# Performance work log

Hardware: AMD Instinct MI355X
Metric: run time of the kernel (lower is better)

Reference implementation:

```python
import jax, jax.numpy as jnp
import numpy as np

N, C = 32768, 1230   # batch of samples, LVIS-scale class count
P = 0.8              # seesaw scale parameter
EPS = 1e-6


def setup_inputs() -> dict:
    key = jax.random.key(0)
    k1, k2, k3 = jax.random.split(key, 3)
    logits = jax.random.normal(k1, (N, C), dtype=jnp.float32)
    labels = jax.random.randint(k2, (N,), 0, C)
    targets = jax.nn.one_hot(labels, C, dtype=jnp.float32)  # one-hot float targets
    # class_counts: long-tailed per-class sample counts (buffer, built in __init__)
    counts = jax.random.randint(k3, (C,), 1, 100000).astype(jnp.float32)
    cond = counts[:, None] > counts[None, :]
    s = jnp.where(cond, (counts[None, :] / counts[:, None]) ** P,
                  jnp.ones((C, C), dtype=jnp.float32))
    return {"logits": logits, "targets": targets, "s": s}


def reference(logits, targets, s):
    # numerically-stable shift (matches torch: logits - max)
    logits = logits - jnp.max(logits, axis=-1, keepdims=True)
    e = jnp.exp(logits)                                   # [N, C]
    # denom[n,i] = sum_j (1 - t[n,j]) * s[i,j] * e[n,j] + e[n,i]
    # original code materializes [N, C, C]; algebraically this is a GEMM:
    denom = jnp.einsum('nj,ij->ni', (1.0 - targets) * e, s) + e
    sigma = e / (denom + EPS)
    loss = -(targets * jnp.log(sigma)).sum(-1)            # [N]
    return loss.mean()
```

## Files before the change

### kernel.cpp

```cpp
#include <hip/hip_runtime.h>
#include <math.h>


constexpr int N_ROWS = 32768;
constexpr int C_CLS  = 1230;
constexpr int C2     = C_CLS / 2;
constexpr int BLK    = 256;
constexpr int PER_T  = (C2 + BLK - 1) / BLK;
constexpr float EPS_F = 1e-6f;

__global__ __launch_bounds__(BLK) void seesaw_row_kernel(
    const float* __restrict__ logits,
    const float* __restrict__ targets,
    const float* __restrict__ s,
    float* __restrict__ row_loss)
{
    const int n    = blockIdx.x;
    const int t    = threadIdx.x;
    const int lane = t & 63;
    const int wv   = t >> 6;

    const float2* lrow = reinterpret_cast<const float2*>(logits  + (size_t)n * C_CLS);
    const float2* trow = reinterpret_cast<const float2*>(targets + (size_t)n * C_CLS);

    __shared__ float red_max[4];
    __shared__ float red_sum[4];
    __shared__ int   sh_label;
    __shared__ float sh_lval;

    float2 l[PER_T];
    float lmax = -INFINITY;
    #pragma unroll
    for (int k = 0; k < PER_T; ++k) {
        const int j2 = t + k * BLK;
        if (j2 < C2) {
            l[k] = lrow[j2];
            const float2 tv = trow[j2];
            lmax = fmaxf(lmax, fmaxf(l[k].x, l[k].y));
            if (tv.x > 0.5f) { sh_label = 2 * j2;     sh_lval = l[k].x; }
            if (tv.y > 0.5f) { sh_label = 2 * j2 + 1; sh_lval = l[k].y; }
        }
    }
    #pragma unroll
    for (int off = 32; off > 0; off >>= 1)
        lmax = fmaxf(lmax, __shfl_down(lmax, off));
    if (lane == 0) red_max[wv] = lmax;
    __syncthreads();
    const float m  = fmaxf(fmaxf(red_max[0], red_max[1]),
                           fmaxf(red_max[2], red_max[3]));
    const int   li = sh_label;
    const float lv = sh_lval;

    const float2* srow = reinterpret_cast<const float2*>(s + (size_t)li * C_CLS);
    const float sii = s[(size_t)li * C_CLS + li];
    float part = 0.0f;
    #pragma unroll
    for (int k = 0; k < PER_T; ++k) {
        const int j2 = t + k * BLK;
        if (j2 < C2) {
            const float2 sv = srow[j2];
            const float ex = expf(l[k].x - m);
            const float ey = expf(l[k].y - m);
            part = fmaf(sv.x, ex, part);
            part = fmaf(sv.y, ey, part);
        }
    }
    #pragma unroll
    for (int off = 32; off > 0; off >>= 1)
        part += __shfl_down(part, off);
    if (lane == 0) red_sum[wv] = part;
    __syncthreads();

    if (t == 0) {
        const float denom_full = red_sum[0] + red_sum[1] + red_sum[2] + red_sum[3];
        const float ei  = expf(lv - m);
        const float denom = denom_full - sii * ei + ei;
        row_loss[n] = logf(denom + EPS_F) - (lv - m);
    }
}

__global__ __launch_bounds__(BLK) void reduce_mean_kernel(
    const float* __restrict__ row_loss, float* __restrict__ out)
{
    const int t    = threadIdx.x;
    const int lane = t & 63;
    const int wv   = t >> 6;
    const float4* rl4 = reinterpret_cast<const float4*>(row_loss);
    constexpr int N4 = N_ROWS / 4;
    double acc = 0.0;
    #pragma unroll 4
    for (int i = t; i < N4; i += BLK) {
        const float4 v = rl4[i];
        acc += (double)v.x + (double)v.y + (double)v.z + (double)v.w;
    }
    #pragma unroll
    for (int off = 32; off > 0; off >>= 1)
        acc += __shfl_down(acc, off);
    __shared__ double red[4];
    if (lane == 0) red[wv] = acc;
    __syncthreads();
    if (t == 0) {
        const double tot = red[0] + red[1] + red[2] + red[3];
        out[0] = (float)(tot / (double)N_ROWS);
    }
}

extern "C" void kernel_launch(void* const* d_in, const int* in_sizes, int n_in,
                              void* d_out, int out_size, void* d_ws, size_t ws_size,
                              hipStream_t stream) {
    const float* logits  = (const float*)d_in[0];
    const float* targets = (const float*)d_in[1];
    const float* s       = (const float*)d_in[2];
    float* out      = (float*)d_out;
    float* row_loss = (float*)d_ws;

    seesaw_row_kernel<<<N_ROWS, BLK, 0, stream>>>(logits, targets, s, row_loss);
    reduce_mean_kernel<<<1, BLK, 0, stream>>>(row_loss, out);
}
```

Baseline: 333.3 us.

## Map one wavefront per row and drop block-level shared-memory reductions

Each 64-lane wavefront now processes a whole row, with four rows per block, so max, label and sum reductions use only xor shuffles with no __syncthreads or shared memory. The label index and value are gathered by summing shuffles (only one lane holds a nonzero), and the label is made wave-uniform with readfirstlane. expf and logf are replaced by the fast __expf and __logf intrinsics. Each lane now holds about 10 float2 values instead of 3, which raises register use and gives less parallelism per row.

```diff
diff --git a/kernel.cpp b/kernel.cpp
--- a/kernel.cpp
+++ b/kernel.cpp
@@ -6,7 +6,8 @@
 constexpr int C_CLS  = 1230;
 constexpr int C2     = C_CLS / 2;
 constexpr int BLK    = 256;
-constexpr int PER_T  = (C2 + BLK - 1) / BLK;
+constexpr int WPB    = BLK / 64;
+constexpr int ITERS  = (C2 + 63) / 64;
 constexpr float EPS_F = 1e-6f;
 
 __global__ __launch_bounds__(BLK) void seesaw_row_kernel(
@@ -15,67 +16,60 @@
     const float* __restrict__ s,
     float* __restrict__ row_loss)
 {
-    const int n    = blockIdx.x;
     const int t    = threadIdx.x;
     const int lane = t & 63;
     const int wv   = t >> 6;
+    const int n    = blockIdx.x * WPB + wv;
 
     const float2* lrow = reinterpret_cast<const float2*>(logits  + (size_t)n * C_CLS);
     const float2* trow = reinterpret_cast<const float2*>(targets + (size_t)n * C_CLS);
 
-    __shared__ float red_max[4];
-    __shared__ float red_sum[4];
-    __shared__ int   sh_label;
-    __shared__ float sh_lval;
+    float2 l[ITERS];
+    float lmax = -INFINITY;
+    float lval = 0.0f;
+    int   li   = 0;
 
-    float2 l[PER_T];
-    float lmax = -INFINITY;
     #pragma unroll
-    for (int k = 0; k < PER_T; ++k) {
-        const int j2 = t + k * BLK;
+    for (int it = 0; it < ITERS; ++it) {
+        const int j2 = lane + it * 64;
         if (j2 < C2) {
-            l[k] = lrow[j2];
+            l[it] = lrow[j2];
             const float2 tv = trow[j2];
-            lmax = fmaxf(lmax, fmaxf(l[k].x, l[k].y));
-            if (tv.x > 0.5f) { sh_label = 2 * j2;     sh_lval = l[k].x; }
-            if (tv.y > 0.5f) { sh_label = 2 * j2 + 1; sh_lval = l[k].y; }
+            lmax = fmaxf(lmax, fmaxf(l[it].x, l[it].y));
+            if (tv.x > 0.5f) { li = 2 * j2;     lval = l[it].x; }
+            if (tv.y > 0.5f) { li = 2 * j2 + 1; lval = l[it].y; }
+        }
+    }
+    #pragma unroll
+    for (int off = 32; off > 0; off >>= 1) {
+        lmax  = fmaxf(lmax, __shfl_xor(lmax, off));
+        li   += __shfl_xor(li, off);
+        lval += __shfl_xor(lval, off);
+    }
+    const int   li_u = __builtin_amdgcn_readfirstlane(li);
+    const float m    = lmax;
+
+    const float2* srow = reinterpret_cast<const float2*>(s + (size_t)li_u * C_CLS);
+    const float sii = s[(size_t)li_u * C_CLS + li_u];
+
+    float part = 0.0f;
+    #pragma unroll
+    for (int it = 0; it < ITERS; ++it) {
+        const int j2 = lane + it * 64;
+        if (j2 < C2) {
+            const float2 sv = srow[j2];
+            part = fmaf(sv.x, __expf(l[it].x - m), part);
+            part = fmaf(sv.y, __expf(l[it].y - m), part);
         }
     }
     #pragma unroll
     for (int off = 32; off > 0; off >>= 1)
-        lmax = fmaxf(lmax, __shfl_down(lmax, off));
-    if (lane == 0) red_max[wv] = lmax;
-    __syncthreads();
-    const float m  = fmaxf(fmaxf(red_max[0], red_max[1]),
-                           fmaxf(red_max[2], red_max[3]));
-    const int   li = sh_label;
-    const float lv = sh_lval;
+        part += __shfl_xor(part, off);
 
-    const float2* srow = reinterpret_cast<const float2*>(s + (size_t)li * C_CLS);
-    const float sii = s[(size_t)li * C_CLS + li];
-    float part = 0.0f;
-    #pragma unroll
-    for (int k = 0; k < PER_T; ++k) {
-        const int j2 = t + k * BLK;
-        if (j2 < C2) {
-            const float2 sv = srow[j2];
-            const float ex = expf(l[k].x - m);
-            const float ey = expf(l[k].y - m);
-            part = fmaf(sv.x, ex, part);
-            part = fmaf(sv.y, ey, part);
-        }
-    }
-    #pragma unroll
-    for (int off = 32; off > 0; off >>= 1)
-        part += __shfl_down(part, off);
-    if (lane == 0) red_sum[wv] = part;
-    __syncthreads();
-
-    if (t == 0) {
-        const float denom_full = red_sum[0] + red_sum[1] + red_sum[2] + red_sum[3];
-        const float ei  = expf(lv - m);
-        const float denom = denom_full - sii * ei + ei;
-        row_loss[n] = logf(denom + EPS_F) - (lv - m);
+    if (lane == 0) {
+        const float ei    = __expf(lval - m);
+        const float denom = part - sii * ei + ei;
+        row_loss[n] = __logf(denom + EPS_F) - (lval - m);
     }
 }
 
@@ -114,6 +108,6 @@
     float* out      = (float*)d_out;
     float* row_loss = (float*)d_ws;
 
-    seesaw_row_kernel<<<N_ROWS, BLK, 0, stream>>>(logits, targets, s, row_loss);
+    seesaw_row_kernel<<<N_ROWS / WPB, BLK, 0, stream>>>(logits, targets, s, row_loss);
     reduce_mean_kernel<<<1, BLK, 0, stream>>>(row_loss, out);
 }
```

Result: no change. 330.4 us (-0.9%).
